# Optimization experiments

Measured on AMD Instinct MI355X. Metric: run time of the kernel, lower is better.

Reference implementation:

```python
import jax, jax.numpy as jnp
import numpy as np

DIM = 256
CTX_DIM = 768
GROUPS = 8
EPS = 1e-5


def setup_inputs() -> dict:
    key = jax.random.key(0)
    ks = jax.random.split(key, 16)
    B, C, H, W, L = 16, DIM, 64, 64, 77
    s_conv = 1.0 / np.sqrt(C * 9)
    s_q = 1.0 / np.sqrt(C)
    s_kv = 1.0 / np.sqrt(CTX_DIM)
    return {
        "x": jax.random.normal(ks[0], (B, C, H, W), jnp.float32),
        "context": jax.random.normal(ks[1], (B, L, CTX_DIM), jnp.float32),
        "conv_w": jax.random.uniform(ks[2], (C, C, 3, 3), jnp.float32, -s_conv, s_conv),
        "conv_b": jax.random.uniform(ks[3], (C,), jnp.float32, -s_conv, s_conv),
        "gn_w": jnp.ones((C,), jnp.float32),
        "gn_b": jnp.zeros((C,), jnp.float32),
        "wq": jax.random.uniform(ks[4], (C, C), jnp.float32, -s_q, s_q),
        "bq": jax.random.uniform(ks[5], (C,), jnp.float32, -s_q, s_q),
        "wk": jax.random.uniform(ks[6], (C, CTX_DIM), jnp.float32, -s_kv, s_kv),
        "bk": jax.random.uniform(ks[7], (C,), jnp.float32, -s_kv, s_kv),
        "wv": jax.random.uniform(ks[8], (C, CTX_DIM), jnp.float32, -s_kv, s_kv),
        "bv": jax.random.uniform(ks[9], (C,), jnp.float32, -s_kv, s_kv),
        "wo": jax.random.uniform(ks[10], (C, C), jnp.float32, -s_q, s_q),
        "bo": jax.random.uniform(ks[11], (C,), jnp.float32, -s_q, s_q),
    }


def _group_norm(h, gn_w, gn_b):
    B, C, H, W = h.shape
    g = h.reshape(B, GROUPS, C // GROUPS, H, W)
    mean = g.mean(axis=(2, 3, 4), keepdims=True)
    var = g.var(axis=(2, 3, 4), keepdims=True)
    g = (g - mean) * jax.lax.rsqrt(var + EPS)
    h = g.reshape(B, C, H, W)
    return h * gn_w[None, :, None, None] + gn_b[None, :, None, None]


def reference(x, context, conv_w, conv_b, gn_w, gn_b, wq, bq, wk, bk, wv, bv, wo, bo):
    B, C, H, W = x.shape
    # conv 3x3, padding=1 (NCHW, OIHW)
    h = jax.lax.conv_general_dilated(
        x, conv_w, window_strides=(1, 1), padding=((1, 1), (1, 1)),
        dimension_numbers=("NCHW", "OIHW", "NCHW"))
    h = h + conv_b[None, :, None, None]
    h = jax.nn.silu(_group_norm(h, gn_w, gn_b))
    # flatten spatial -> tokens: [B, HW, C]
    hf = h.reshape(B, C, H * W).transpose(0, 2, 1)
    q = hf @ wq.T + bq                     # [B, HW, C]
    k = context @ wk.T + bk                # [B, L, C]
    v = context @ wv.T + bv                # [B, L, C]
    scale = 1.0 / jnp.sqrt(jnp.asarray(C, q.dtype))
    att = jax.nn.softmax(jnp.einsum("bqc,bkc->bqk", q, k) * scale, axis=-1)
    o = jnp.einsum("bqk,bkc->bqc", att, v) @ wo.T + bo
    h_att = o.transpose(0, 2, 1).reshape(B, C, H, W)
    return x + h_att
```

## Files before the change

kernel.cpp:

```cpp
#include <hip/hip_runtime.h>
#include <stdint.h>

#define B_  16
#define C_  256
#define HW_ 4096
#define Hp  66
#define PP  4356
#define EPS_ 1e-5f

typedef unsigned short u16;
typedef unsigned int   u32;
typedef __attribute__((ext_vector_type(4))) float  f32x4;
typedef __attribute__((ext_vector_type(8))) __bf16 bf16x8;
typedef __attribute__((ext_vector_type(8))) u16    u16x8;

__device__ __forceinline__ float bf2f(u16 u){ u32 x = ((u32)u)<<16; float f; __builtin_memcpy(&f,&x,4); return f; }
__device__ __forceinline__ u16 f2bf(float f){ u32 x; __builtin_memcpy(&x,&f,4); u32 r = x + 0x7fffu + ((x>>16)&1u); return (u16)(r>>16); }

__device__ __forceinline__ void g2l16(const void* g, void* l){
  __builtin_amdgcn_global_load_lds((__attribute__((address_space(1))) void*)(void*)g,
                                   (__attribute__((address_space(3))) void*)l, 16, 0, 0);
}
__device__ __forceinline__ bf16x8 ldfrag(const u16* p){
  u16x8 r = *(const u16x8*)p;
  return __builtin_bit_cast(bf16x8, r);
}

__global__ __launch_bounds__(256) void k_pad(const float* __restrict__ x, u16* __restrict__ xpT){
  int bid = blockIdx.x; int b = bid/66, hh = bid - b*66; int tid = threadIdx.x;
  u16* rowbase = xpT + (size_t)(b*PP + hh*Hp)*C_;
  if(hh==0 || hh==65){
    u32* p = (u32*)rowbase;
    for(int i=tid;i<66*C_/2;i+=256) p[i]=0u;
    return;
  }
  if(tid<128) ((u32*)rowbase)[tid]=0u;
  else ((u32*)(rowbase + 65*C_))[tid-128]=0u;
  int h = hh-1;
  __shared__ float Lt[64*65];
  for(int cc=0; cc<4; cc++){
    int c0=cc*64;
    int ci = tid>>2, w0 = (tid&3)*16;
    const float* xs = x + ((size_t)(b*C_ + c0+ci)*HW_) + h*64 + w0;
    for(int j=0;j<4;j++){
      float4 v = *(const float4*)(xs + j*4);
      Lt[ci*65 + w0 + j*4 + 0] = v.x;
      Lt[ci*65 + w0 + j*4 + 1] = v.y;
      Lt[ci*65 + w0 + j*4 + 2] = v.z;
      Lt[ci*65 + w0 + j*4 + 3] = v.w;
    }
    __syncthreads();
    int w = tid>>2, cj = (tid&3)*16;
    union { u16 u[16]; uint4 v[2]; } outu;
    for(int j=0;j<16;j++) outu.u[j] = f2bf(Lt[(cj+j)*65 + w]);
    uint4* dst = (uint4*)(rowbase + (size_t)(w+1)*C_ + c0 + cj);
    dst[0]=outu.v[0]; dst[1]=outu.v[1];
    __syncthreads();
  }
}

__global__ __launch_bounds__(256) void k_repack(
    const float* __restrict__ conv_w, const float* __restrict__ wq, const float* __restrict__ wo,
    const float* __restrict__ wk, const float* __restrict__ wv, const float* __restrict__ ctx,
    u16* __restrict__ wBt, u16* __restrict__ wqB, u16* __restrict__ woB,
    u16* __restrict__ wkvB, u16* __restrict__ ctxB, float* __restrict__ stats){
  int i = blockIdx.x*256 + threadIdx.x;
  if(i < 589824){ int co = i/2304, k = i - co*2304; int t = k>>8, ci = k&255;
    wBt[i] = f2bf(conv_w[(co*256+ci)*9 + t]); return; }
  i -= 589824;
  if(i < 65536){ wqB[i] = f2bf(wq[i]); return; } i -= 65536;
  if(i < 65536){ woB[i] = f2bf(wo[i]); return; } i -= 65536;
  if(i < 196608){ wkvB[i] = f2bf(wk[i]); return; } i -= 196608;
  if(i < 196608){ wkvB[196608+i] = f2bf(wv[i]); return; } i -= 196608;
  if(i < 946176){ ctxB[i] = f2bf(ctx[i]); return; } i -= 946176;
  if(i < 512){ stats[i] = 0.f; }
}

__global__ __launch_bounds__(256, 2) void k_conv(const u16* __restrict__ xpT, const u16* __restrict__ wBt,
    const float* __restrict__ conv_b, u16* __restrict__ h, float* __restrict__ stats){
  __shared__ u16 As[264*32];
  __shared__ u16 Bs[256*32];
  int bid = blockIdx.x;
  int b = bid >> 5, hp = bid & 31;
  int tid = threadIdx.x;
  int w = tid>>6, lane = tid&63, ln = lane&15, qd = lane>>4;
  int wm = w&1, wn = w>>1;
  const u16* Abase = xpT + (size_t)(b*PP + hp*132)*C_;
  f32x4 acc[4][8] = {};
  int hr_[4], wp_[4];
  #pragma unroll
  for(int mf=0;mf<4;mf++){ int p = wm*64 + mf*16 + ln; hr_[mf] = p>>6; wp_[mf] = p&63; }

  for(int ci=0; ci<8; ci++){
    int ci0 = ci*32;
    #pragma unroll
    for(int r=0;r<5;r++){
      int c = r*256 + tid;
      if(c < 1056){
        int ipix = c>>2, atom = c&3;
        g2l16(Abase + (size_t)ipix*C_ + ci0 + atom*8, &As[c*8]);
      }
    }
    for(int t=0;t<9;t++){
      int dy = (t*11)>>5, dx = t - dy*3;
      #pragma unroll
      for(int r=0;r<4;r++){
        int c = r*256 + tid;
        int co = c>>2, atom = c&3;
        g2l16(wBt + (size_t)co*2304 + t*256 + ci0 + atom*8, &Bs[c*8]);
      }
      __syncthreads();
      bf16x8 af[4], bfv[8];
      #pragma unroll
      for(int mf=0;mf<4;mf++){
        int ipix = (hr_[mf]+dy)*66 + wp_[mf] + dx;
        af[mf] = ldfrag(&As[ipix*32 + qd*8]);
      }
      #pragma unroll
      for(int nf=0;nf<8;nf++) bfv[nf] = ldfrag(&Bs[(wn*128+nf*16+ln)*32 + qd*8]);
      #pragma unroll
      for(int mf=0;mf<4;mf++)
        #pragma unroll
        for(int nf=0;nf<8;nf++)
          acc[mf][nf] = __builtin_amdgcn_mfma_f32_16x16x32_bf16(af[mf], bfv[nf], acc[mf][nf], 0,0,0);
      __syncthreads();
    }
  }
  float s[4]={0,0,0,0}, q[4]={0,0,0,0};
  int p0 = hp*128;
  for(int nf=0;nf<8;nf++){
    int n = wn*128 + nf*16 + ln;
    float bias = conv_b[n];
    for(int mf=0;mf<4;mf++){
      for(int r=0;r<4;r++){
        int p = wm*64 + mf*16 + qd*4 + r;
        float v = acc[mf][nf][r] + bias;
        h[((size_t)(b*HW_ + p0 + p))*C_ + n] = f2bf(v);
        s[nf>>1]+=v; q[nf>>1]+=v*v;
      }
    }
  }
  for(int off=32;off>=1;off>>=1){
    #pragma unroll
    for(int g=0;g<4;g++){ s[g]+=__shfl_down(s[g],off,64); q[g]+=__shfl_down(q[g],off,64); }
  }
  if(lane==0){
    #pragma unroll
    for(int g=0;g<4;g++){
      atomicAdd(&stats[(b*8 + wn*4 + g)*2+0], s[g]);
      atomicAdd(&stats[(b*8 + wn*4 + g)*2+1], q[g]);
    }
  }
}

__global__ __launch_bounds__(256, 2) void k_qgn(const u16* __restrict__ hbuf, const u16* __restrict__ wqB,
    const float* __restrict__ stats, const float* __restrict__ gnw, const float* __restrict__ gnb,
    const float* __restrict__ bq, u16* __restrict__ qb){
  __shared__ u16 As[128*32];
  __shared__ u16 Bs[256*32];
  int mt = blockIdx.x;
  int b = mt >> 5;
  int tid = threadIdx.x;
  int w = tid>>6, lane = tid&63, ln = lane&15, qd = lane>>4;
  int wm = w&1, wn = w>>1;
  int pr = tid>>1, half = tid&1;
  const u16* hsrc = hbuf + ((size_t)(mt*128+pr))*256 + half*16;
  f32x4 acc[4][8] = {};
  uint4 ra0, ra1, rb0, rb1;
  ra0 = *(const uint4*)(hsrc);
  ra1 = *(const uint4*)(hsrc + 8);
  for(int kt=0; kt<8; kt++){
    float sm = stats[(b*8+kt)*2], qm = stats[(b*8+kt)*2+1];
    float mean = sm*(1.f/131072.f);
    float rstd = rsqrtf(qm*(1.f/131072.f) - mean*mean + EPS_);
    int c0 = kt*32 + half*16;
    float4 gw0 = *(const float4*)(gnw+c0), gw1 = *(const float4*)(gnw+c0+4);
    float4 gw2 = *(const float4*)(gnw+c0+8), gw3 = *(const float4*)(gnw+c0+12);
    float4 gb0 = *(const float4*)(gnb+c0), gb1 = *(const float4*)(gnb+c0+4);
    float4 gb2 = *(const float4*)(gnb+c0+8), gb3 = *(const float4*)(gnb+c0+12);
    float gwv[16] = {gw0.x,gw0.y,gw0.z,gw0.w, gw1.x,gw1.y,gw1.z,gw1.w,
                     gw2.x,gw2.y,gw2.z,gw2.w, gw3.x,gw3.y,gw3.z,gw3.w};
    float gbv[16] = {gb0.x,gb0.y,gb0.z,gb0.w, gb1.x,gb1.y,gb1.z,gb1.w,
                     gb2.x,gb2.y,gb2.z,gb2.w, gb3.x,gb3.y,gb3.z,gb3.w};
    u16 inu[16];
    ((uint4*)inu)[0] = ra0; ((uint4*)inu)[1] = ra1;
    u16 outu[16];
    #pragma unroll
    for(int j=0;j<16;j++){
      float v = bf2f(inu[j]);
      v = (v-mean)*rstd*gwv[j] + gbv[j];
      float s = v/(1.f+__expf(-v));
      outu[j] = f2bf(s);
    }
    u16* adst = &As[pr*32 + half*16];
    ((uint4*)adst)[0] = ((uint4*)outu)[0];
    ((uint4*)adst)[1] = ((uint4*)outu)[1];
    #pragma unroll
    for(int r=0;r<4;r++){
      int c = r*256 + tid;
      int co = c>>2, atom = c&3;
      g2l16(wqB + (size_t)co*256 + kt*32 + atom*8, &Bs[c*8]);
    }
    if(kt<7){
      rb0 = *(const uint4*)(hsrc + (kt+1)*32);
      rb1 = *(const uint4*)(hsrc + (kt+1)*32 + 8);
    }
    __syncthreads();
    bf16x8 af[4], bfv[8];
    #pragma unroll
    for(int mf=0;mf<4;mf++) af[mf] = ldfrag(&As[(wm*64+mf*16+ln)*32 + qd*8]);
    #pragma unroll
    for(int nf=0;nf<8;nf++) bfv[nf] = ldfrag(&Bs[(wn*128+nf*16+ln)*32 + qd*8]);
    #pragma unroll
    for(int mf=0;mf<4;mf++)
      #pragma unroll
      for(int nf=0;nf<8;nf++)
        acc[mf][nf] = __builtin_amdgcn_mfma_f32_16x16x32_bf16(af[mf], bfv[nf], acc[mf][nf], 0,0,0);
    __syncthreads();
    ra0 = rb0; ra1 = rb1;
  }
  for(int nf=0;nf<8;nf++){
    int n = wn*128 + nf*16 + ln;
    float bias = bq[n];
    for(int mf=0;mf<4;mf++){
      for(int r=0;r<4;r++){
        int ml = wm*64 + mf*16 + qd*4 + r;
        qb[((size_t)(mt*128+ml))*256 + n] = f2bf(acc[mf][nf][r]+bias);
      }
    }
  }
}

__global__ __launch_bounds__(256) void k_kvproj(const u16* __restrict__ ctxB, const u16* __restrict__ wkvB,
    const float* __restrict__ bk, const float* __restrict__ bv,
    u16* __restrict__ kb, u16* __restrict__ vT){
  __shared__ u16 As[64*128];
  __shared__ u16 Bs[64*128];
  int bid = blockIdx.x;
  int nt = bid & 7, mt = bid >> 3;
  int n0 = nt*64, m0 = mt*64;
  int tid=threadIdx.x, w=tid>>6, lane=tid&63, ln=lane&15, qd=lane>>4;
  int wm = w&1, wn = w>>1;
  f32x4 acc[2][2]={};
  for(int kt=0;kt<6;kt++){
    #pragma unroll
    for(int r=0;r<4;r++){
      int c = r*256 + tid;
      int row = c>>4, atom = c&15;
      g2l16(ctxB + ((size_t)(m0+row)*768 + kt*128 + atom*8), &As[c*8]);
      g2l16(wkvB + ((size_t)(n0+row)*768 + kt*128 + atom*8), &Bs[c*8]);
    }
    __syncthreads();
    #pragma unroll
    for(int kk=0;kk<4;kk++){
      bf16x8 af[2], bfv[2];
      #pragma unroll
      for(int mf=0;mf<2;mf++) af[mf]=ldfrag(&As[(wm*32+mf*16+ln)*128 + kk*32 + qd*8]);
      #pragma unroll
      for(int nf=0;nf<2;nf++) bfv[nf]=ldfrag(&Bs[(wn*32+nf*16+ln)*128 + kk*32 + qd*8]);
      #pragma unroll
      for(int mf=0;mf<2;mf++)
        #pragma unroll
        for(int nf=0;nf<2;nf++)
          acc[mf][nf]=__builtin_amdgcn_mfma_f32_16x16x32_bf16(af[mf],bfv[nf],acc[mf][nf],0,0,0);
    }
    __syncthreads();
  }
  for(int mf=0;mf<2;mf++) for(int nf=0;nf<2;nf++){
    int ng = n0 + wn*32 + nf*16 + ln;
    float bias = ng<256 ? bk[ng] : bv[ng-256];
    for(int r=0;r<4;r++){
      int mg = m0 + wm*32 + mf*16 + qd*4 + r;
      if(mg<1232){
        float v=acc[mf][nf][r]+bias;
        int bb=mg/77, l=mg-bb*77;
        if(ng<256) kb[((size_t)(bb*77+l))*256+ng]=f2bf(v);
        else vT[((size_t)(bb*256+(ng-256)))*96 + l]=f2bf(v);
      }
    }
  }
}

__global__ __launch_bounds__(256) void k_attn(const u16* __restrict__ qg, const u16* __restrict__ kb,
    const u16* __restrict__ vT, u16* __restrict__ ob){
  __shared__ u16 Qs[4096];
  __shared__ u16 KVs[4096];
  __shared__ u16 Sb[128*84];
  __shared__ u16 Pb[128*104];
  int bid=blockIdx.x; int b=bid>>5, qt=bid&31; int p0=qt*128;
  int tid=threadIdx.x, w=tid>>6, lane=tid&63, ln=lane&15, qd=lane>>4;
  int srow=tid>>2, koff=(tid&3)*8;
  f32x4 Sa[2][5]={};
  for(int kt=0;kt<8;kt++){
    for(int j=0;j<2;j++){
      int m=srow+j*64;
      g2l16(qg + ((size_t)(b*HW_+p0+m)*256 + kt*32+koff), &Qs[(size_t)tid*8+j*2048]);
    }
    for(int j=0;j<2;j++){
      int cja = tid + j*256;
      if(cja < 320){
        int l = cja>>2, ko2=(cja&3)*8;
        g2l16(kb + ((size_t)(b*77+l)*256 + kt*32+ko2), &KVs[(size_t)cja*8]);
      }
    }
    __syncthreads();
    bf16x8 af[2], bfv[5];
    for(int mf=0;mf<2;mf++) af[mf]=ldfrag(&Qs[(w*32+mf*16+ln)*32+qd*8]);
    for(int nf=0;nf<5;nf++) bfv[nf]=ldfrag(&KVs[(nf*16+ln)*32+qd*8]);
    for(int mf=0;mf<2;mf++) for(int nf=0;nf<5;nf++)
      Sa[mf][nf]=__builtin_amdgcn_mfma_f32_16x16x32_bf16(af[mf],bfv[nf],Sa[mf][nf],0,0,0);
    __syncthreads();
  }
  for(int mf=0;mf<2;mf++) for(int nf=0;nf<5;nf++) for(int r=0;r<4;r++){
    int ml=w*32+mf*16+qd*4+r, nl=nf*16+ln;
    Sb[ml*84+nl]=f2bf(Sa[mf][nf][r]*0.0625f);
  }
  __syncthreads();
  if(tid<128){
    const u16* srp = &Sb[tid*84];
    u16* prow = &Pb[tid*104];
    float mx=-1e30f;
    for(int j2=0;j2<77;j2++){ float v=bf2f(srp[j2]); mx=fmaxf(mx,v); }
    float sum=0.f;
    for(int j2=0;j2<77;j2++){ float e=__expf(bf2f(srp[j2])-mx); sum+=e; prow[j2]=f2bf(e); }
    float inv=1.f/sum;
    for(int j2=0;j2<77;j2++){ prow[j2]=f2bf(bf2f(prow[j2])*inv); }
    for(int j2=77;j2<104;j2++) prow[j2]=0;
  }
  __syncthreads();
  for(int nh=0;nh<2;nh++){
    f32x4 Oa[2][8]={};
    for(int kt2=0;kt2<3;kt2++){
      for(int j=0;j<2;j++){
        int chunk=tid+j*256;
        int co=chunk>>2, ko2=(chunk&3)*8;
        g2l16(vT + ((size_t)(b*256+nh*128+co)*96 + kt2*32+ko2), &KVs[(size_t)chunk*8]);
      }
      __syncthreads();
      bf16x8 af[2], bfv[8];
      for(int mf=0;mf<2;mf++) af[mf]=ldfrag(&Pb[(w*32+mf*16+ln)*104 + kt2*32+qd*8]);
      for(int nf=0;nf<8;nf++) bfv[nf]=ldfrag(&KVs[(nf*16+ln)*32+qd*8]);
      for(int mf=0;mf<2;mf++) for(int nf=0;nf<8;nf++)
        Oa[mf][nf]=__builtin_amdgcn_mfma_f32_16x16x32_bf16(af[mf],bfv[nf],Oa[mf][nf],0,0,0);
      __syncthreads();
    }
    for(int mf=0;mf<2;mf++) for(int nf=0;nf<8;nf++) for(int r=0;r<4;r++){
      int ml=w*32+mf*16+qd*4+r, nl=nh*128+nf*16+ln;
      ob[((size_t)(b*HW_+p0+ml))*256+nl]=f2bf(Oa[mf][nf][r]);
    }
  }
}

__global__ __launch_bounds__(256) void k_oproj(const u16* __restrict__ ob, const u16* __restrict__ woB,
    const float* __restrict__ bo, const float* __restrict__ x, float* __restrict__ outp){
  __shared__ u16 As[128*32];
  __shared__ u16 Bs[128*32];
  int bid=blockIdx.x;
  int b=bid>>6; int rr=bid&63; int cm=rr>>5, pt=rr&31;
  int c0=cm*128, p0=pt*128;
  int tid=threadIdx.x, w=tid>>6, lane=tid&63, ln=lane&15, qd=lane>>4, wm=w>>1, wn=w&1;
  int srow=tid>>2, koff=(tid&3)*8;
  f32x4 acc[4][4]={};
  for(int kt=0;kt<8;kt++){
    for(int j=0;j<2;j++){
      int m=srow+j*64;
      g2l16(woB + ((size_t)(c0+m)*256 + kt*32+koff),        &As[(size_t)tid*8+j*2048]);
      g2l16(ob  + ((size_t)(b*HW_+p0+m)*256 + kt*32+koff),  &Bs[(size_t)tid*8+j*2048]);
    }
    __syncthreads();
    bf16x8 af[4], bfv[4];
    for(int mf=0;mf<4;mf++) af[mf]=ldfrag(&As[(wm*64+mf*16+ln)*32+qd*8]);
    for(int nf=0;nf<4;nf++) bfv[nf]=ldfrag(&Bs[(wn*64+nf*16+ln)*32+qd*8]);
    for(int mf=0;mf<4;mf++) for(int nf=0;nf<4;nf++)
      acc[mf][nf]=__builtin_amdgcn_mfma_f32_16x16x32_bf16(af[mf],bfv[nf],acc[mf][nf],0,0,0);
    __syncthreads();
  }
  for(int mf=0;mf<4;mf++) for(int r=0;r<4;r++){
    int cl=c0+wm*64+mf*16+qd*4+r;
    float bias=bo[cl];
    for(int nf=0;nf<4;nf++){
      int pl=p0+wn*64+nf*16+ln;
      size_t idx=((size_t)(b*C_+cl))*HW_+pl;
      outp[idx]=x[idx]+acc[mf][nf][r]+bias;
    }
  }
}

extern "C" void kernel_launch(void* const* d_in, const int* in_sizes, int n_in,
                              void* d_out, int out_size, void* d_ws, size_t ws_size,
                              hipStream_t stream){
  const float* x      = (const float*)d_in[0];
  const float* ctx    = (const float*)d_in[1];
  const float* conv_w = (const float*)d_in[2];
  const float* conv_b = (const float*)d_in[3];
  const float* gnw    = (const float*)d_in[4];
  const float* gnb    = (const float*)d_in[5];
  const float* wq     = (const float*)d_in[6];
  const float* bq     = (const float*)d_in[7];
  const float* wk     = (const float*)d_in[8];
  const float* bk     = (const float*)d_in[9];
  const float* wv     = (const float*)d_in[10];
  const float* bv     = (const float*)d_in[11];
  const float* wo     = (const float*)d_in[12];
  const float* bo     = (const float*)d_in[13];
  char* ws = (char*)d_ws;
  u16* xpT  = (u16*)(ws + 0);
  u16* wBt  = (u16*)(ws + 35684352);
  u16* wqB  = (u16*)(ws + 36864000);
  u16* wkvB = (u16*)(ws + 36995072);
  u16* woB  = (u16*)(ws + 37781504);
  u16* ctxB = (u16*)(ws + 37912576);
  u16* hbuf = (u16*)(ws + 39804928);
  u16* kbv  = (u16*)(ws + 73359360);
  u16* vT   = (u16*)(ws + 73990144);
  u16* obuf = (u16*)(ws + 74776576);
  float* stats = (float*)(ws + 108331008);
  u16* qb = xpT;
  float* outp = (float*)d_out;

  k_pad   <<<1056, 256, 0, stream>>>(x, xpT);
  k_repack<<<8050, 256, 0, stream>>>(conv_w, wq, wo, wk, wv, ctx, wBt, wqB, woB, wkvB, ctxB, stats);
  k_conv  <<<512,  256, 0, stream>>>(xpT, wBt, conv_b, hbuf, stats);
  k_qgn   <<<512,  256, 0, stream>>>(hbuf, wqB, stats, gnw, gnb, bq, qb);
  k_kvproj<<<160,  256, 0, stream>>>(ctxB, wkvB, bk, bv, kbv, vT);
  k_attn  <<<512,  256, 0, stream>>>(qb, kbv, vT, obuf);
  k_oproj <<<1024, 256, 0, stream>>>(obuf, woB, bo, x, outp);
}
```

Before: 382.3 us.

## Double-buffer conv weight tiles via register prefetch with padded LDS rows

Measured after the change: 669.0 us. +75.0%, slower.

```diff
diff --git a/kernel.cpp b/kernel.cpp
--- a/kernel.cpp
+++ b/kernel.cpp
@@ -78,8 +78,8 @@
 
 __global__ __launch_bounds__(256, 2) void k_conv(const u16* __restrict__ xpT, const u16* __restrict__ wBt,
     const float* __restrict__ conv_b, u16* __restrict__ h, float* __restrict__ stats){
-  __shared__ u16 As[264*32];
-  __shared__ u16 Bs[256*32];
+  __shared__ u16 As[264*36];
+  __shared__ u16 Bs[2][256*36];
   int bid = blockIdx.x;
   int b = bid >> 5, hp = bid & 31;
   int tid = threadIdx.x;
@@ -90,40 +90,83 @@
   int hr_[4], wp_[4];
   #pragma unroll
   for(int mf=0;mf<4;mf++){ int p = wm*64 + mf*16 + ln; hr_[mf] = p>>6; wp_[mf] = p&63; }
-
+  const u16* bsrc[4]; int bofs[4];
+  #pragma unroll
+  for(int r=0;r<4;r++){
+    int c = r*256 + tid; int co = c>>2, at = c&3;
+    bsrc[r] = wBt + (size_t)co*2304 + at*8;
+    bofs[r] = co*36 + at*8;
+  }
+  const u16* asrc[5]; int aofs[5];
+  #pragma unroll
+  for(int r=0;r<5;r++){
+    int c = r*256 + tid; int row = c>>2, at = c&3;
+    asrc[r] = Abase + (size_t)row*C_ + at*8;
+    aofs[r] = row*36 + at*8;
+  }
+  bool a4 = (tid < 32);
+
+  uint4 rb[4], ra[5];
+  #pragma unroll
+  for(int r=0;r<4;r++) ra[r] = *(const uint4*)(asrc[r]);
+  if(a4) ra[4] = *(const uint4*)(asrc[4]);
+  #pragma unroll
+  for(int r=0;r<4;r++) rb[r] = *(const uint4*)(bsrc[r]);
+  #pragma unroll
+  for(int r=0;r<4;r++) *(uint4*)(&As[aofs[r]]) = ra[r];
+  if(a4) *(uint4*)(&As[aofs[4]]) = ra[4];
+  #pragma unroll
+  for(int r=0;r<4;r++) *(uint4*)(&Bs[0][bofs[r]]) = rb[r];
+  #pragma unroll
+  for(int r=0;r<4;r++) rb[r] = *(const uint4*)(bsrc[r] + 256);
+  __syncthreads();
+
+  int cb = 0;
+  int tL = 2, ciL = 0;
   for(int ci=0; ci<8; ci++){
-    int ci0 = ci*32;
-    #pragma unroll
-    for(int r=0;r<5;r++){
-      int c = r*256 + tid;
-      if(c < 1056){
-        int ipix = c>>2, atom = c&3;
-        g2l16(Abase + (size_t)ipix*C_ + ci0 + atom*8, &As[c*8]);
-      }
-    }
     for(int t=0;t<9;t++){
+      int s = ci*9 + t;
+      if(s < 71){
+        #pragma unroll
+        for(int r=0;r<4;r++) *(uint4*)(&Bs[cb^1][bofs[r]]) = rb[r];
+        if(s < 70){
+          int off = tL*256 + ciL*32;
+          #pragma unroll
+          for(int r=0;r<4;r++) rb[r] = *(const uint4*)(bsrc[r] + off);
+          if(++tL == 9){ tL = 0; ciL++; }
+        }
+      }
+      if(t==7 && ci<7){
+        int off = (ci+1)*32;
+        #pragma unroll
+        for(int r=0;r<4;r++) ra[r] = *(const uint4*)(asrc[r] + off);
+        if(a4) ra[4] = *(const uint4*)(asrc[4] + off);
+      }
       int dy = (t*11)>>5, dx = t - dy*3;
-      #pragma unroll
-      for(int r=0;r<4;r++){
-        int c = r*256 + tid;
-        int co = c>>2, atom = c&3;
-        g2l16(wBt + (size_t)co*2304 + t*256 + ci0 + atom*8, &Bs[c*8]);
-      }
-      __syncthreads();
       bf16x8 af[4], bfv[8];
       #pragma unroll
       for(int mf=0;mf<4;mf++){
         int ipix = (hr_[mf]+dy)*66 + wp_[mf] + dx;
-        af[mf] = ldfrag(&As[ipix*32 + qd*8]);
-      }
-      #pragma unroll
-      for(int nf=0;nf<8;nf++) bfv[nf] = ldfrag(&Bs[(wn*128+nf*16+ln)*32 + qd*8]);
+        af[mf] = ldfrag(&As[ipix*36 + qd*8]);
+      }
+      #pragma unroll
+      for(int nf=0;nf<8;nf++){
+        int n = wn*128 + nf*16 + ln;
+        bfv[nf] = ldfrag(&Bs[cb][n*36 + qd*8]);
+      }
       #pragma unroll
       for(int mf=0;mf<4;mf++)
         #pragma unroll
         for(int nf=0;nf<8;nf++)
           acc[mf][nf] = __builtin_amdgcn_mfma_f32_16x16x32_bf16(af[mf], bfv[nf], acc[mf][nf], 0,0,0);
       __syncthreads();
+      if(t==8 && ci<7){
+        #pragma unroll
+        for(int r=0;r<4;r++) *(uint4*)(&As[aofs[r]]) = ra[r];
+        if(a4) *(uint4*)(&As[aofs[4]]) = ra[4];
+        __syncthreads();
+      }
+      cb ^= 1;
     }
   }
   float s[4]={0,0,0,0}, q[4]={0,0,0,0};
```
